# Performance work log

Measured on AMD Instinct MI355X. Metric: run time of the kernel, lower is better.

The kernel has to match this reference:

```python
import jax, jax.numpy as jnp
import numpy as np

NUM_HEADS = 8


def setup_inputs() -> dict:
    key = jax.random.key(0)
    ks = jax.random.split(key, 7)
    B, D, N = 16, 512, 2048
    sc = 1.0 / np.sqrt(D)
    return {
        "X_Query": jax.random.normal(ks[0], (B, D, N), jnp.float32),
        "X_Key": jax.random.normal(ks[1], (B, D, N), jnp.float32),
        "X_Value": jax.random.normal(ks[2], (B, D, N), jnp.float32),
        "W_q": jax.random.normal(ks[3], (D, D), jnp.float32) * sc,
        "W_k": jax.random.normal(ks[4], (D, D), jnp.float32) * sc,
        "W_v": jax.random.normal(ks[5], (D, D), jnp.float32) * sc,
        "W_o": jax.random.normal(ks[6], (D, D), jnp.float32) * sc,
    }


def _proj(W, x):
    # Conv1d(D, D, kernel_size=1, bias=False) == channel matmul
    return jnp.einsum('oi,bin->bon', W, x)


def _split_heads(x, h):
    # torch: cat(x.chunk(h, dim=-1), dim=0) -> (h, B, D, N/h) stacked layout
    B, D, N = x.shape
    return x.reshape(B, D, h, N // h).transpose(2, 0, 1, 3)


def _mha(XQ, XK, XV, Wq, Wk, Wv, Wo):
    B, D, N = XQ.shape
    h = NUM_HEADS
    Nh = N // h
    q = _split_heads(_proj(Wq, XQ), h)  # (h, B, D, Nh)
    k = _split_heads(_proj(Wk, XK), h)
    v = _split_heads(_proj(Wv, XV), h)
    # scores over the CHANNEL axis: (h, B, D, D), scaled by sqrt(d_k)=sqrt(Nh)
    scores = jnp.einsum('hbdn,hben->hbde', q, k) / jnp.sqrt(jnp.asarray(Nh, q.dtype))
    p = jax.nn.softmax(scores, axis=-1)
    out = jnp.einsum('hbde,hben->hbdn', p, v)  # (h, B, D, Nh)
    # torch: cat(chunks, dim=0) inverse -> cat along dim=-1
    attn_heads = out.transpose(1, 2, 0, 3).reshape(B, D, N)
    return _proj(Wo, XQ - attn_heads)


def reference(X_Query, X_Key, X_Value, W_q, W_k, W_v, W_o):
    return _mha(X_Query, X_Key, X_Value, W_q, W_k, W_v, W_o)
```

## Files before the change

kernel.cpp:

```cpp
#include <hip/hip_runtime.h>
#include <hip/hip_bf16.h>

#define DD  512
#define NN  2048
#define BB  16
#define NHD 256

typedef unsigned short u16;
typedef __attribute__((ext_vector_type(4))) float f32x4;
typedef __attribute__((ext_vector_type(8))) short s16x8;
typedef __attribute__((ext_vector_type(4))) u16   u16x4;

static __device__ __forceinline__ u16 f2bf(float f) {
  __hip_bfloat16 h = __float2bfloat16(f);
  return *reinterpret_cast<u16*>(&h);
}
static __device__ __forceinline__ float bf2f(u16 u) {
  union { unsigned int i; float f; } v; v.i = ((unsigned int)u) << 16; return v.f;
}
static __device__ __forceinline__ f32x4 mfma_bf16(s16x8 a, s16x8 b, f32x4 c) {
  return __builtin_amdgcn_mfma_f32_16x16x32_bf16(a, b, c, 0, 0, 0);
}
static __device__ __forceinline__ void gload_lds16(const u16* g, u16* l) {
  __builtin_amdgcn_global_load_lds(
      (const __attribute__((address_space(1))) unsigned int*)g,
      (__attribute__((address_space(3))) unsigned int*)l, 16, 0, 0);
}

__global__ __launch_bounds__(256) void k_cvt_w(const float* __restrict__ w0,
                                               const float* __restrict__ w1,
                                               const float* __restrict__ w2,
                                               const float* __restrict__ w3,
                                               u16* __restrict__ out) {
  const float* srcs[4] = {w0, w1, w2, w3};
  const float* s = srcs[blockIdx.y];
  u16* o = out + (size_t)blockIdx.y * (DD * DD);
  int idx = blockIdx.x * 256 + threadIdx.x;
  float4 v = *(const float4*)(s + (size_t)idx * 4);
  u16x4 u = {f2bf(v.x), f2bf(v.y), f2bf(v.z), f2bf(v.w)};
  *(u16x4*)(o + (size_t)idx * 4) = u;
}

__global__ __launch_bounds__(256) void k_transpose(const float* __restrict__ X,
                                                   u16* __restrict__ XT) {
  __shared__ float t[64][68];
  const int tid = threadIdx.x;
  const int n0 = blockIdx.x * 64, d0 = blockIdx.y * 64, b = blockIdx.z;
  const float* Xb = X + ((size_t)b * DD + d0) * NN + n0;
#pragma unroll
  for (int i = 0; i < 4; ++i) {
    int r = (tid >> 4) + i * 16;
    int c = (tid & 15) * 4;
    float4 v = *(const float4*)(Xb + (size_t)r * NN + c);
    t[r][c] = v.x; t[r][c + 1] = v.y; t[r][c + 2] = v.z; t[r][c + 3] = v.w;
  }
  __syncthreads();
  u16* Ob = XT + ((size_t)b * NN + n0) * DD + d0;
#pragma unroll
  for (int i = 0; i < 4; ++i) {
    int n = (tid >> 4) + i * 16;
    int d = (tid & 15) * 4;
    u16x4 u = {f2bf(t[d][n]), f2bf(t[d + 1][n]), f2bf(t[d + 2][n]), f2bf(t[d + 3][n])};
    *(u16x4*)(Ob + (size_t)n * DD + d) = u;
  }
}

#define GEMM_STAGE(Ag, lda, Bg, ldb, buf, kt)                                   \
  {                                                                             \
    _Pragma("unroll")                                                           \
    for (int j = 0; j < 4; ++j) {                                               \
      int s = j * 256 + w * 64 + lane;                                          \
      int row = s >> 3, u = s & 7;                                              \
      int col = ((u ^ (row & 7)) * 8);                                          \
      gload_lds16(Ag + (size_t)row * lda + (kt) * 64 + col, &Ab[buf][s * 8]);   \
      gload_lds16(Bg + (size_t)row * ldb + (kt) * 64 + col, &Bb[buf][s * 8]);   \
    }                                                                           \
  }

#define GEMM_COMPUTE(buf)                                                       \
  {                                                                             \
    _Pragma("unroll")                                                           \
    for (int ks = 0; ks < 2; ++ks) {                                            \
      s16x8 av[4], bv[4];                                                       \
      _Pragma("unroll")                                                         \
      for (int m = 0; m < 4; ++m) {                                             \
        int row = wm + m * 16 + r;                                              \
        av[m] = *(const s16x8*)&Ab[buf][row * 64 + (((ks * 4 + g) ^ (row & 7)) * 8)]; \
      }                                                                         \
      _Pragma("unroll")                                                         \
      for (int nf = 0; nf < 4; ++nf) {                                          \
        int row = wn + nf * 16 + r;                                             \
        bv[nf] = *(const s16x8*)&Bb[buf][row * 64 + (((ks * 4 + g) ^ (row & 7)) * 8)]; \
      }                                                                         \
      _Pragma("unroll")                                                         \
      for (int m = 0; m < 4; ++m)                                               \
        _Pragma("unroll")                                                       \
        for (int nf = 0; nf < 4; ++nf)                                          \
          acc[m][nf] = mfma_bf16(av[m], bv[nf], acc[m][nf]);                    \
    }                                                                           \
  }

#define GEMM_PREAMBLE                                                           \
  __shared__ __align__(16) u16 Ab[2][128 * 64];                                 \
  __shared__ __align__(16) u16 Bb[2][128 * 64];                                 \
  const int tid = threadIdx.x;                                                  \
  const int lane = tid & 63, w = tid >> 6;                                      \
  const int wm = (w >> 1) * 64, wn = (w & 1) * 64;                              \
  const int r = lane & 15, g = lane >> 4;                                       \
  f32x4 acc[4][4] = {};

#define GEMM_MAINLOOP(Ag, lda, Bg, ldb, nkt)                                    \
  GEMM_STAGE(Ag, lda, Bg, ldb, 0, 0);                                           \
  __syncthreads();                                                              \
  for (int kt = 0; kt < (nkt) - 1; ++kt) {                                      \
    GEMM_STAGE(Ag, lda, Bg, ldb, (kt & 1) ^ 1, kt + 1);                         \
    GEMM_COMPUTE(kt & 1);                                                       \
    __syncthreads();                                                            \
  }                                                                             \
  GEMM_COMPUTE(((nkt) - 1) & 1);

template <typename OUT_T>
__global__ __launch_bounds__(256) void k_gemm_nt(
    const u16* __restrict__ A, long long a_bs, int lda,
    const u16* __restrict__ B, long long b_bs, int ldb,
    OUT_T* __restrict__ C, long long c_bs, int ldc, int K) {
  GEMM_PREAMBLE
  const int m0 = blockIdx.x * 128, n0 = blockIdx.y * 128;
  const u16* Ag = A + (size_t)blockIdx.z * a_bs + (size_t)m0 * lda;
  const u16* Bg = B + (size_t)blockIdx.z * b_bs + (size_t)n0 * ldb;
  const int nkt = K >> 6;
  GEMM_MAINLOOP(Ag, lda, Bg, ldb, nkt);

  OUT_T* Cg = C + (size_t)blockIdx.z * c_bs;
#pragma unroll
  for (int m = 0; m < 4; ++m)
#pragma unroll
    for (int nf = 0; nf < 4; ++nf)
#pragma unroll
      for (int j = 0; j < 4; ++j) {
        int row = m0 + wm + m * 16 + g * 4 + j;
        int col = n0 + wn + nf * 16 + r;
        float v = acc[m][nf][j];
        if constexpr (sizeof(OUT_T) == 2) Cg[(size_t)row * ldc + col] = f2bf(v);
        else                              Cg[(size_t)row * ldc + col] = v;
      }
}

__global__ __launch_bounds__(256) void k_gemm_p(const u16* __restrict__ Qdn,
                                                const u16* __restrict__ Kdn,
                                                u16* __restrict__ P,
                                                float* __restrict__ rs_part) {
  GEMM_PREAMBLE
  const int m0 = blockIdx.x * 128, n0 = blockIdx.y * 128;
  const int hb = blockIdx.z, b = hb >> 3, h = hb & 7;
  const u16* Ag = Qdn + ((size_t)b * DD + m0) * NN + h * NHD;
  const u16* Bg = Kdn + ((size_t)b * DD + n0) * NN + h * NHD;
  GEMM_MAINLOOP(Ag, NN, Bg, NN, 4);

  u16* Pg = P + (size_t)hb * DD * DD;
  float* rsg = rs_part + ((size_t)hb * DD) * 8 + blockIdx.y * 2 + (wn >> 6);
#pragma unroll
  for (int m = 0; m < 4; ++m)
#pragma unroll
    for (int j = 0; j < 4; ++j) {
      const int row = m0 + wm + m * 16 + g * 4 + j;
      float s = 0.f;
#pragma unroll
      for (int nf = 0; nf < 4; ++nf) {
        const int col = n0 + wn + nf * 16 + r;
        float p = __expf(acc[m][nf][j] * 0.0625f);
        s += p;
        Pg[(size_t)row * DD + col] = f2bf(p);
      }
      s += __shfl_xor(s, 1);
      s += __shfl_xor(s, 2);
      s += __shfl_xor(s, 4);
      s += __shfl_xor(s, 8);
      if (r == 0) rsg[(size_t)row * 8] = s;
    }
}

__global__ __launch_bounds__(256) void k_gemm_pv(const u16* __restrict__ VT,
                                                 const u16* __restrict__ P,
                                                 const float* __restrict__ rs_part,
                                                 const u16* __restrict__ XqT,
                                                 u16* __restrict__ And) {
  GEMM_PREAMBLE
  const int m0 = blockIdx.x * 128, n0 = blockIdx.y * 128;
  const int hb = blockIdx.z, b = hb >> 3, h = hb & 7;
  const u16* Ag = VT + ((size_t)b * NN + h * NHD + m0) * DD;
  const u16* Bg = P + (size_t)hb * DD * DD + (size_t)n0 * DD;
  GEMM_MAINLOOP(Ag, DD, Bg, DD, 8);

  const float* rsg = rs_part + (size_t)hb * DD * 8;
  const size_t base = ((size_t)b * NN + h * NHD + m0) * DD;
  const u16* Xg = XqT + base;
  u16* Og = And + base;
#pragma unroll
  for (int nf = 0; nf < 4; ++nf) {
    const int col = n0 + wn + nf * 16 + r;
    float rs = 0.f;
#pragma unroll
    for (int t = 0; t < 8; ++t) rs += rsg[(size_t)col * 8 + t];
    const float inv = 1.0f / rs;
#pragma unroll
    for (int m = 0; m < 4; ++m)
#pragma unroll
      for (int j = 0; j < 4; ++j) {
        const int row = wm + m * 16 + g * 4 + j;
        float val = acc[m][nf][j] * inv;
        float xq = bf2f(Xg[(size_t)row * DD + col]);
        Og[(size_t)row * DD + col] = f2bf(xq - val);
      }
  }
}

extern "C" void kernel_launch(void* const* d_in, const int* in_sizes, int n_in,
                              void* d_out, int out_size, void* d_ws, size_t ws_size,
                              hipStream_t stream) {
  const float* Xq = (const float*)d_in[0];
  const float* Xk = (const float*)d_in[1];
  const float* Xv = (const float*)d_in[2];
  const float* Wq = (const float*)d_in[3];
  const float* Wk = (const float*)d_in[4];
  const float* Wv = (const float*)d_in[5];
  const float* Wo = (const float*)d_in[6];
  float* out = (float*)d_out;

  char* ws = (char*)d_ws;
  const size_t MB = 1024 * 1024;
  u16* Wb  = (u16*)ws;
  u16* XqT = (u16*)(ws + 2 * MB);
  u16* Z2  = (u16*)(ws + 34 * MB);
  u16* Pb  = (u16*)(ws + 34 * MB);
  u16* Qdn = (u16*)(ws + 98 * MB);
  u16* And = (u16*)(ws + 98 * MB);
  float* rs_part = (float*)(ws + 130 * MB);
  u16* VTb = (u16*)d_out;
  u16* Kdn = (u16*)d_out + (size_t)BB * NN * DD;

  k_cvt_w<<<dim3(256, 4), 256, 0, stream>>>(Wq, Wk, Wv, Wo, Wb);

  k_transpose<<<dim3(NN / 64, DD / 64, BB), 256, 0, stream>>>(Xv, Z2);
  k_gemm_nt<u16><<<dim3(NN / 128, DD / 128, BB), 256, 0, stream>>>(
      Z2, (long long)NN * DD, DD,
      Wb + 2 * DD * DD, 0, DD,
      VTb, (long long)NN * DD, DD, DD);

  k_transpose<<<dim3(NN / 64, DD / 64, BB), 256, 0, stream>>>(Xq, XqT);
  k_gemm_nt<u16><<<dim3(DD / 128, NN / 128, BB), 256, 0, stream>>>(
      Wb, 0, DD,
      XqT, (long long)NN * DD, DD,
      Qdn, (long long)DD * NN, NN, DD);

  k_transpose<<<dim3(NN / 64, DD / 64, BB), 256, 0, stream>>>(Xk, Z2);
  k_gemm_nt<u16><<<dim3(DD / 128, NN / 128, BB), 256, 0, stream>>>(
      Wb + 1 * DD * DD, 0, DD,
      Z2, (long long)NN * DD, DD,
      Kdn, (long long)DD * NN, NN, DD);

  k_gemm_p<<<dim3(4, 4, BB * 8), 256, 0, stream>>>(Qdn, Kdn, Pb, rs_part);

  k_gemm_pv<<<dim3(2, 4, BB * 8), 256, 0, stream>>>(VTb, Pb, rs_part, XqT, And);

  k_gemm_nt<float><<<dim3(DD / 128, NN / 128, BB), 256, 0, stream>>>(
      Wb + 3 * DD * DD, 0, DD,
      And, (long long)NN * DD, DD,
      out, (long long)DD * NN, NN, DD);
}
```

Measured before the change: 291.5 us.

## Fuse score, softmax and PV GEMMs into one flash-style attention kernel

Replaces the separate score-GEMM (writing the bf16 exp-scores P and partial row sums to global memory) and PV-GEMM with a single fused kernel. Each 512-thread block owns 128 query channels for one head and batch, keeps Q fragments in registers, and streams K and V tiles through double-buffered LDS. It exponentiates scores into an LDS P tile and accumulates P·V directly, normalising by row sums at the end. This removes the global round trip of P (16·8·512·512 bf16) and the rs_part buffer, at the cost of fewer blocks (512), heavier LDS use and more barriers per block.

```diff
diff --git a/kernel.cpp b/kernel.cpp
--- a/kernel.cpp
+++ b/kernel.cpp
@@ -146,73 +146,165 @@
       }
 }
 
-__global__ __launch_bounds__(256) void k_gemm_p(const u16* __restrict__ Qdn,
-                                                const u16* __restrict__ Kdn,
-                                                u16* __restrict__ P,
-                                                float* __restrict__ rs_part) {
-  GEMM_PREAMBLE
-  const int m0 = blockIdx.x * 128, n0 = blockIdx.y * 128;
-  const int hb = blockIdx.z, b = hb >> 3, h = hb & 7;
-  const u16* Ag = Qdn + ((size_t)b * DD + m0) * NN + h * NHD;
-  const u16* Bg = Kdn + ((size_t)b * DD + n0) * NN + h * NHD;
-  GEMM_MAINLOOP(Ag, NN, Bg, NN, 4);
-
-  u16* Pg = P + (size_t)hb * DD * DD;
-  float* rsg = rs_part + ((size_t)hb * DD) * 8 + blockIdx.y * 2 + (wn >> 6);
-#pragma unroll
-  for (int m = 0; m < 4; ++m)
+__global__ __launch_bounds__(512, 2) void k_attn_fused(
+    const u16* __restrict__ Qdn, const u16* __restrict__ Kdn,
+    const u16* __restrict__ VT,  const u16* __restrict__ XqT,
+    u16* __restrict__ And) {
+  __shared__ __align__(16) u16 Ks[2][128 * 64];
+  __shared__ __align__(16) u16 Vs[2][256 * 64];
+  __shared__ __align__(16) u16 Ps[128 * 128];
+  __shared__ float rs_lds[8][32];
+  __shared__ float rs_inv[128];
+
+  const int tid = threadIdx.x;
+  const int lane = tid & 63, w = tid >> 6;
+  const int r = lane & 15, g = lane >> 4;
+  const int wq = w >> 1, wn1 = w & 1;
+  const int bid = blockIdx.x;
+  const int h = bid & 7, dt = (bid >> 3) & 3, b = bid >> 5;
+  const int d0 = dt * 128, hn0 = h * NHD;
+
+  const u16* Qg = Qdn + ((size_t)b * DD + d0) * NN + hn0;
+  const u16* Kg = Kdn + ((size_t)b * DD) * NN + hn0;
+  const u16* Vg = VT + ((size_t)b * NN + hn0) * DD;
+  u16* Qst = (u16*)Vs;
+
+  auto stage_k = [&](int idx) {
+    const int et = idx >> 2, ks = idx & 3, buf = idx & 1;
+#pragma unroll
+    for (int j = 0; j < 2; ++j) {
+      int s = j * 512 + tid;
+      int row = s >> 3, u = s & 7;
+      gload_lds16(Kg + (size_t)(et * 128 + row) * NN + ks * 64 + ((u ^ (row & 7)) * 8),
+                  &Ks[buf][s * 8]);
+    }
+  };
+  auto stage_v = [&](int et, int vs) {
 #pragma unroll
     for (int j = 0; j < 4; ++j) {
-      const int row = m0 + wm + m * 16 + g * 4 + j;
-      float s = 0.f;
-#pragma unroll
-      for (int nf = 0; nf < 4; ++nf) {
-        const int col = n0 + wn + nf * 16 + r;
-        float p = __expf(acc[m][nf][j] * 0.0625f);
-        s += p;
-        Pg[(size_t)row * DD + col] = f2bf(p);
+      int s = j * 512 + tid;
+      int row = s >> 3, u = s & 7;
+      gload_lds16(Vg + (size_t)row * DD + et * 128 + vs * 64 + ((u ^ (row & 7)) * 8),
+                  &Vs[vs][s * 8]);
+    }
+  };
+
+  stage_k(0);
+#pragma unroll
+  for (int j = 0; j < 8; ++j) {
+    int s = j * 512 + tid;
+    int row = s >> 5, u = s & 31;
+    gload_lds16(Qg + (size_t)row * NN + ((u ^ (row & 7)) * 8), &Qst[s * 8]);
+  }
+  __syncthreads();
+  s16x8 qf[2][8];
+#pragma unroll
+  for (int ms = 0; ms < 2; ++ms)
+#pragma unroll
+    for (int k2 = 0; k2 < 8; ++k2) {
+      int row = wq * 32 + ms * 16 + r;
+      qf[ms][k2] = *(const s16x8*)&Qst[row * 256 + (((k2 * 4 + g) ^ (row & 7)) * 8)];
+    }
+  __syncthreads();
+
+  float psum[2][4] = {};
+  f32x4 acc_o[4][4] = {};
+
+  for (int et = 0; et < 4; ++et) {
+    f32x4 acc_s[2][4] = {};
+#pragma unroll
+    for (int ks = 0; ks < 4; ++ks) {
+      const int idx = et * 4 + ks;
+      if (idx + 1 < 16) stage_k(idx + 1);
+      if (ks == 2) stage_v(et, 0);
+      if (ks == 3) stage_v(et, 1);
+      const int buf = idx & 1;
+#pragma unroll
+      for (int kq = 0; kq < 2; ++kq) {
+        s16x8 bv[4];
+#pragma unroll
+        for (int nf = 0; nf < 4; ++nf) {
+          int row = wn1 * 64 + nf * 16 + r;
+          bv[nf] = *(const s16x8*)&Ks[buf][row * 64 + (((kq * 4 + g) ^ (row & 7)) * 8)];
+        }
+#pragma unroll
+        for (int ms = 0; ms < 2; ++ms)
+#pragma unroll
+          for (int nf = 0; nf < 4; ++nf)
+            acc_s[ms][nf] = mfma_bf16(qf[ms][ks * 2 + kq], bv[nf], acc_s[ms][nf]);
       }
-      s += __shfl_xor(s, 1);
-      s += __shfl_xor(s, 2);
-      s += __shfl_xor(s, 4);
-      s += __shfl_xor(s, 8);
-      if (r == 0) rsg[(size_t)row * 8] = s;
-    }
-}
-
-__global__ __launch_bounds__(256) void k_gemm_pv(const u16* __restrict__ VT,
-                                                 const u16* __restrict__ P,
-                                                 const float* __restrict__ rs_part,
-                                                 const u16* __restrict__ XqT,
-                                                 u16* __restrict__ And) {
-  GEMM_PREAMBLE
-  const int m0 = blockIdx.x * 128, n0 = blockIdx.y * 128;
-  const int hb = blockIdx.z, b = hb >> 3, h = hb & 7;
-  const u16* Ag = VT + ((size_t)b * NN + h * NHD + m0) * DD;
-  const u16* Bg = P + (size_t)hb * DD * DD + (size_t)n0 * DD;
-  GEMM_MAINLOOP(Ag, DD, Bg, DD, 8);
-
-  const float* rsg = rs_part + (size_t)hb * DD * 8;
-  const size_t base = ((size_t)b * NN + h * NHD + m0) * DD;
-  const u16* Xg = XqT + base;
-  u16* Og = And + base;
-#pragma unroll
-  for (int nf = 0; nf < 4; ++nf) {
-    const int col = n0 + wn + nf * 16 + r;
-    float rs = 0.f;
-#pragma unroll
-    for (int t = 0; t < 8; ++t) rs += rsg[(size_t)col * 8 + t];
-    const float inv = 1.0f / rs;
-#pragma unroll
-    for (int m = 0; m < 4; ++m)
+      __syncthreads();
+    }
+#pragma unroll
+    for (int ms = 0; ms < 2; ++ms)
+#pragma unroll
+      for (int nf = 0; nf < 4; ++nf)
+#pragma unroll
+        for (int j = 0; j < 4; ++j) {
+          int rowd = wq * 32 + ms * 16 + g * 4 + j;
+          int cole = wn1 * 64 + nf * 16 + r;
+          float p = __expf(acc_s[ms][nf][j] * 0.0625f);
+          psum[ms][j] += p;
+          *(u16*)((char*)Ps + rowd * 256 + ((cole * 2) ^ ((rowd & 7) << 4))) = f2bf(p);
+        }
+    __syncthreads();
+#pragma unroll
+    for (int vs = 0; vs < 2; ++vs) {
+#pragma unroll
+      for (int kss = 0; kss < 2; ++kss) {
+        s16x8 pb[4];
+#pragma unroll
+        for (int nf = 0; nf < 4; ++nf) {
+          int rowd = wn1 * 64 + nf * 16 + r;
+          pb[nf] = *(const s16x8*)((char*)Ps + rowd * 256 +
+                                   (((vs * 64 + kss * 32 + g * 8) * 2) ^ ((rowd & 7) << 4)));
+        }
+#pragma unroll
+        for (int ms = 0; ms < 4; ++ms) {
+          int rown = wq * 64 + ms * 16 + r;
+          s16x8 av = *(const s16x8*)&Vs[vs][rown * 64 + (((kss * 4 + g) ^ (rown & 7)) * 8)];
+#pragma unroll
+          for (int nf = 0; nf < 4; ++nf)
+            acc_o[ms][nf] = mfma_bf16(av, pb[nf], acc_o[ms][nf]);
+        }
+      }
+    }
+  }
+
+#pragma unroll
+  for (int ms = 0; ms < 2; ++ms)
+#pragma unroll
+    for (int j = 0; j < 4; ++j) {
+      float v = psum[ms][j];
+      v += __shfl_xor(v, 1);
+      v += __shfl_xor(v, 2);
+      v += __shfl_xor(v, 4);
+      v += __shfl_xor(v, 8);
+      if (r == 0) rs_lds[w][ms * 16 + g * 4 + j] = v;
+    }
+  __syncthreads();
+  if (tid < 128) {
+    int q = tid >> 5, idx = tid & 31;
+    rs_inv[tid] = 1.0f / (rs_lds[q * 2][idx] + rs_lds[q * 2 + 1][idx]);
+  }
+  __syncthreads();
+
+  const u16* Xg = XqT + ((size_t)b * NN + hn0) * DD + d0;
+  u16* Ag = And + ((size_t)b * NN + hn0) * DD + d0;
+#pragma unroll
+  for (int ms = 0; ms < 4; ++ms)
+#pragma unroll
+    for (int nf = 0; nf < 4; ++nf) {
+      const int dc = wn1 * 64 + nf * 16 + r;
+      const float inv = rs_inv[dc];
 #pragma unroll
       for (int j = 0; j < 4; ++j) {
-        const int row = wm + m * 16 + g * 4 + j;
-        float val = acc[m][nf][j] * inv;
-        float xq = bf2f(Xg[(size_t)row * DD + col]);
-        Og[(size_t)row * DD + col] = f2bf(xq - val);
+        const int npos = wq * 64 + ms * 16 + g * 4 + j;
+        float o = acc_o[ms][nf][j] * inv;
+        float xq = bf2f(Xg[(size_t)npos * DD + dc]);
+        Ag[(size_t)npos * DD + dc] = f2bf(xq - o);
       }
-  }
+    }
 }
 
 extern "C" void kernel_launch(void* const* d_in, const int* in_sizes, int n_in,
@@ -232,10 +324,8 @@
   u16* Wb  = (u16*)ws;
   u16* XqT = (u16*)(ws + 2 * MB);
   u16* Z2  = (u16*)(ws + 34 * MB);
-  u16* Pb  = (u16*)(ws + 34 * MB);
-  u16* Qdn = (u16*)(ws + 98 * MB);
-  u16* And = (u16*)(ws + 98 * MB);
-  float* rs_part = (float*)(ws + 130 * MB);
+  u16* And = Z2;
+  u16* Qdn = (u16*)(ws + 66 * MB);
   u16* VTb = (u16*)d_out;
   u16* Kdn = (u16*)d_out + (size_t)BB * NN * DD;
 
@@ -259,9 +349,7 @@
       Z2, (long long)NN * DD, DD,
       Kdn, (long long)DD * NN, NN, DD);
 
-  k_gemm_p<<<dim3(4, 4, BB * 8), 256, 0, stream>>>(Qdn, Kdn, Pb, rs_part);
-
-  k_gemm_pv<<<dim3(2, 4, BB * 8), 256, 0, stream>>>(VTb, Pb, rs_part, XqT, And);
+  k_attn_fused<<<dim3(512), 512, 0, stream>>>(Qdn, Kdn, VTb, XqT, And);
 
   k_gemm_nt<float><<<dim3(DD / 128, NN / 128, BB), 256, 0, stream>>>(
       Wb + 3 * DD * DD, 0, DD,
```

After: 264.9 us. 1.1x faster.
